# Kernel tuning notes

Measured on AMD Instinct MI355X. Metric: run time of the kernel, lower is better.

Reference implementation:

```python
import math
import jax, jax.numpy as jnp
import numpy as np

B, S, H = 4, 4096, 1024
NH, HD = 16, 64
MLP_DIM = 4096


def _gelu_tanh(x):
    c = math.sqrt(2.0 / math.pi)
    return 0.5 * x * (1.0 + jnp.tanh(c * (x + 0.044715 * x * x * x)))


def _layernorm(x, w, b, eps=1e-5):
    mu = jnp.mean(x, axis=-1, keepdims=True)
    var = jnp.var(x, axis=-1, keepdims=True)
    return (x - mu) * jax.lax.rsqrt(var + eps) * w + b


def setup_inputs() -> dict:
    key = jax.random.key(0)
    ks = jax.random.split(key, 12)
    s = 0.02
    return {
        "x": jax.random.normal(ks[0], (B, S, H), jnp.float32),
        "ln1_w": jnp.ones((H,), jnp.float32),
        "ln1_b": jnp.zeros((H,), jnp.float32),
        "q_w": jax.random.normal(ks[1], (H, H), jnp.float32) * s,
        "q_b": jnp.zeros((H,), jnp.float32),
        "k_w": jax.random.normal(ks[2], (H, H), jnp.float32) * s,
        "k_b": jnp.zeros((H,), jnp.float32),
        "v_w": jax.random.normal(ks[3], (H, H), jnp.float32) * s,
        "v_b": jnp.zeros((H,), jnp.float32),
        "o_w": jax.random.normal(ks[4], (H, H), jnp.float32) * s,
        "o_b": jnp.zeros((H,), jnp.float32),
        "ln2_w": jnp.ones((H,), jnp.float32),
        "ln2_b": jnp.zeros((H,), jnp.float32),
        "fc_w": jax.random.normal(ks[5], (H, MLP_DIM), jnp.float32) * s,
        "fc_b": jnp.zeros((MLP_DIM,), jnp.float32),
        "proj_w": jax.random.normal(ks[6], (MLP_DIM, H), jnp.float32) * (s / math.sqrt(2 * 12)),
        "proj_b": jnp.zeros((H,), jnp.float32),
    }


def reference(x, ln1_w, ln1_b, q_w, q_b, k_w, k_b, v_w, v_b, o_w, o_b,
              ln2_w, ln2_b, fc_w, fc_b, proj_w, proj_b):
    bsz, seqlen, h = x.shape
    ln_x = _layernorm(x, ln1_w, ln1_b)

    # projections -> [b, nh, t, hd]
    def heads(y):
        return y.reshape(bsz, seqlen, NH, HD).transpose(0, 2, 1, 3)

    q = heads(ln_x @ q_w + q_b)
    k = heads(ln_x @ k_w + k_b)
    v = heads(ln_x @ v_w + v_b)

    # feature map: elu(x)+1
    qf = jax.nn.elu(q) + 1.0
    kf = jax.nn.elu(k) + 1.0

    kv = jnp.einsum('bhtd,bhte->bhde', kf, v)              # [b,nh,hd,hd]
    norm = 1.0 / (jnp.einsum('bhtd,bhd->bht', qf, kf.sum(axis=2)) + 1e-6)
    out = jnp.einsum('bhtd,bhde->bhte', qf, kv) * norm[..., None]
    out = out.transpose(0, 2, 1, 3).reshape(bsz, seqlen, h)
    attn = out @ o_w + o_b

    x = x + attn
    h_mlp = _gelu_tanh(_layernorm(x, ln2_w, ln2_b) @ fc_w + fc_b)
    x = x + (h_mlp @ proj_w + proj_b)
    return x
```

## Files before the change

### kernel.cpp

```cpp
#include <hip/hip_runtime.h>
#include <hip/hip_bf16.h>
#include <cstdint>
#include <cstddef>

typedef __bf16 bf16;
typedef __bf16 bf16x8 __attribute__((ext_vector_type(8)));
typedef __bf16 bf16x4 __attribute__((ext_vector_type(4)));
typedef float  f32x4  __attribute__((ext_vector_type(4)));

typedef __attribute__((address_space(1))) void gvoid_t;
typedef __attribute__((address_space(3))) void lvoid_t;

#define GLD_LDS16(g, l) __builtin_amdgcn_global_load_lds( \
    (gvoid_t*)(uintptr_t)(g), (lvoid_t*)(uint32_t)(uintptr_t)(l), 16, 0, 0)

#define SBAR() __builtin_amdgcn_s_barrier()
#define SCHED_FENCE() __builtin_amdgcn_sched_barrier(0)
#define WAIT_VMN(n) asm volatile("s_waitcnt vmcnt(" #n ")" ::: "memory")
#define WAIT_LGKM0() asm volatile("s_waitcnt lgkmcnt(0)" ::: "memory")

__global__ __launch_bounds__(256) void transpose_cast(
    const float* __restrict__ in, bf16* __restrict__ out, int R, int C)
{
  __shared__ float tile[32][33];
  const int bx = blockIdx.x;
  const int by = blockIdx.y;
  const int tx = threadIdx.x;
  const int ty = threadIdx.y;
#pragma unroll
  for (int i = 0; i < 32; i += 8)
    tile[ty + i][tx] = in[(size_t)(by * 32 + ty + i) * C + bx * 32 + tx];
  __syncthreads();
#pragma unroll
  for (int i = 0; i < 32; i += 8)
    out[(size_t)(bx * 32 + ty + i) * R + by * 32 + tx] = (bf16)tile[tx][ty + i];
}

__global__ __launch_bounds__(256) void pack3(
    const float* __restrict__ a, const float* __restrict__ b,
    const float* __restrict__ c, float* __restrict__ o)
{
  const int i = blockIdx.x * 256 + threadIdx.x;
  o[i] = i < 1024 ? a[i] : (i < 2048 ? b[i - 1024] : c[i - 2048]);
}

__global__ __launch_bounds__(256) void ln_row(
    const float* __restrict__ x, const float* __restrict__ w,
    const float* __restrict__ b, bf16* __restrict__ out)
{
  const int row = blockIdx.x;
  const int tid = threadIdx.x;
  const float4 v = ((const float4*)(x + (size_t)row * 1024))[tid];
  float s  = v.x + v.y + v.z + v.w;
  float ss = v.x * v.x + v.y * v.y + v.z * v.z + v.w * v.w;
#pragma unroll
  for (int off = 32; off > 0; off >>= 1) {
    s  += __shfl_down(s, off);
    ss += __shfl_down(ss, off);
  }
  __shared__ float red[8];
  const int wid = tid >> 6, lane = tid & 63;
  if (lane == 0) { red[wid] = s; red[4 + wid] = ss; }
  __syncthreads();
  s  = red[0] + red[1] + red[2] + red[3];
  ss = red[4] + red[5] + red[6] + red[7];
  const float mu   = s * (1.f / 1024.f);
  const float var  = ss * (1.f / 1024.f) - mu * mu;
  const float rstd = rsqrtf(var + 1e-5f);
  const float4 wv = ((const float4*)w)[tid];
  const float4 bv = ((const float4*)b)[tid];
  bf16x4 ov;
  ov[0] = (bf16)((v.x - mu) * rstd * wv.x + bv.x);
  ov[1] = (bf16)((v.y - mu) * rstd * wv.y + bv.y);
  ov[2] = (bf16)((v.z - mu) * rstd * wv.z + bv.z);
  ov[3] = (bf16)((v.w - mu) * rstd * wv.w + bv.w);
  *(bf16x4*)(out + (size_t)row * 1024 + tid * 4) = ov;
}

template <int EPI>
__global__ __launch_bounds__(512, 2) void gemm256(
    const bf16* __restrict__ A, const bf16* __restrict__ BT,
    const float* __restrict__ bias, const float* __restrict__ resid,
    void* __restrict__ outp, int M, int N, int K, int nx)
{
  __shared__ __align__(16) char lds[131072];
  const int tid  = threadIdx.x;
  const int wid  = tid >> 6, lane = tid & 63;
  const int wr   = wid >> 2, wc = wid & 3;
  const int ln15 = lane & 15, lhi = lane >> 4;

  const int nwg = (int)gridDim.x;
  const int cpx = nwg >> 3;
  const int bid = (int)blockIdx.x;
  const int lg  = (bid & 7) * cpx + (bid >> 3);
  const int bx  = lg % nx, by = lg / nx;
  const int row0 = by << 8, col0 = bx << 8;

  const int srowA = tid >> 3;
  const int sslA  = (tid & 7) ^ (srowA & 7);
  const bf16* aS  = A + (size_t)(row0 + srowA) * K + sslA * 8;
  const size_t rjK = (size_t)K << 6;
  const int u8    = tid >> 3, s8 = tid & 7;
  const int gRowB = ((u8 >> 5) << 6) + (u8 & 31);
  const int sslB  = s8 ^ (u8 & 7);
  const bf16* bS  = BT + (size_t)(col0 + gRowB) * K + sslB * 8;

  char* ldsAw = lds + wid * 1024;
  char* ldsBw = lds + 65536 + wid * 1024;

  const int slk0 = (lhi ^ (ln15 & 7)) << 4;
  const int slk1 = ((4 + lhi) ^ (ln15 & 7)) << 4;
  const int rowA0 = ((wr << 7) + ln15) * 128;
  const int rowB0 = 65536 + (wc * 32 + ln15) * 128;

  f32x4 acc[8][4] = {};
  bf16x8 a[4][2], b0[2][2], b1[2][2];
  const int nt = K >> 6;

#define STG_A(D, KT, I) GLD_LDS16(aS + (size_t)(I) * rjK + (size_t)(KT) * 64, \
                                  ldsAw + (D) * 32768 + (I) * 8192)
#define STG_B(D, KT, NH, J) GLD_LDS16(bS + (size_t)((J) * 128 + (NH) * 32) * K + (size_t)(KT) * 64, \
                                      ldsBw + (D) * 32768 + (NH) * 16384 + (J) * 8192)
#define RD_A(D, MH) do { _Pragma("unroll") \
    for (int m_ = 0; m_ < 4; ++m_) { \
      a[m_][0] = *(const bf16x8*)(lds + (D) * 32768 + rowA0 + (MH) * 8192 + m_ * 2048 + slk0); \
      a[m_][1] = *(const bf16x8*)(lds + (D) * 32768 + rowA0 + (MH) * 8192 + m_ * 2048 + slk1); \
    } } while (0)
#define RD_B(D, NH, DST) do { _Pragma("unroll") \
    for (int n_ = 0; n_ < 2; ++n_) { \
      DST[n_][0] = *(const bf16x8*)(lds + (D) * 32768 + rowB0 + (NH) * 16384 + n_ * 2048 + slk0); \
      DST[n_][1] = *(const bf16x8*)(lds + (D) * 32768 + rowB0 + (NH) * 16384 + n_ * 2048 + slk1); \
    } } while (0)
#define MFMA8(MH, NH, BSRC) do { \
    __builtin_amdgcn_s_setprio(1); \
    _Pragma("unroll") for (int m_ = 0; m_ < 4; ++m_) \
    _Pragma("unroll") for (int n_ = 0; n_ < 2; ++n_) { \
      acc[(MH) * 4 + m_][(NH) * 2 + n_] = __builtin_amdgcn_mfma_f32_16x16x32_bf16( \
          a[m_][0], BSRC[n_][0], acc[(MH) * 4 + m_][(NH) * 2 + n_], 0, 0, 0); \
      acc[(MH) * 4 + m_][(NH) * 2 + n_] = __builtin_amdgcn_mfma_f32_16x16x32_bf16( \
          a[m_][1], BSRC[n_][1], acc[(MH) * 4 + m_][(NH) * 2 + n_], 0, 0, 0); \
    } \
    __builtin_amdgcn_s_setprio(0); } while (0)

  STG_A(0, 0, 0); STG_A(0, 0, 2);
  STG_B(0, 0, 0, 0); STG_B(0, 0, 0, 1);
  STG_B(0, 0, 1, 0); STG_B(0, 0, 1, 1);
  STG_A(0, 0, 1); STG_A(0, 0, 3);
  WAIT_VMN(0);
  SBAR(); SCHED_FENCE();

  for (int kt = 0; kt < nt - 1; ++kt) {
    const int d = kt & 1, dn = d ^ 1;
    RD_A(d, 0); RD_B(d, 0, b0);
    STG_A(dn, kt + 1, 0); STG_A(dn, kt + 1, 2);
    SBAR(); WAIT_LGKM0(); SCHED_FENCE();
    MFMA8(0, 0, b0);
    SBAR(); SCHED_FENCE();
    RD_B(d, 1, b1);
    STG_B(dn, kt + 1, 0, 0); STG_B(dn, kt + 1, 0, 1);
    WAIT_VMN(4);
    SBAR(); WAIT_LGKM0(); SCHED_FENCE();
    MFMA8(0, 1, b1);
    SBAR(); SCHED_FENCE();
    RD_A(d, 1);
    STG_B(dn, kt + 1, 1, 0); STG_B(dn, kt + 1, 1, 1);
    SBAR(); WAIT_LGKM0(); SCHED_FENCE();
    MFMA8(1, 0, b0);
    SBAR(); SCHED_FENCE();
    STG_A(dn, kt + 1, 1); STG_A(dn, kt + 1, 3);
    MFMA8(1, 1, b1);
    WAIT_VMN(2);
    SBAR(); SCHED_FENCE();
  }

  {
    const int d = (nt - 1) & 1;
    RD_A(d, 0); RD_B(d, 0, b0);
    SBAR(); WAIT_LGKM0(); SCHED_FENCE();
    MFMA8(0, 0, b0);
    SBAR(); SCHED_FENCE();
    RD_B(d, 1, b1);
    WAIT_VMN(0);
    SBAR(); WAIT_LGKM0(); SCHED_FENCE();
    MFMA8(0, 1, b1);
    SBAR(); SCHED_FENCE();
    RD_A(d, 1);
    WAIT_LGKM0(); SCHED_FENCE();
    MFMA8(1, 0, b0);
    MFMA8(1, 1, b1);
  }
#undef STG_A
#undef STG_B
#undef RD_A
#undef RD_B
#undef MFMA8

  const int lr4 = lhi << 2;
#pragma unroll
  for (int m = 0; m < 8; ++m) {
#pragma unroll
    for (int n = 0; n < 4; ++n) {
      const int c_i = col0 + wc * 64 + n * 16 + ln15;
      const float bv = bias[c_i];
#pragma unroll
      for (int j = 0; j < 4; ++j) {
        const int r_i = row0 + wr * 128 + m * 16 + lr4 + j;
        const size_t idx = (size_t)r_i * N + c_i;
        float val = acc[m][n][j] + bv;
        if constexpr (EPI == 0) {
          ((bf16*)outp)[idx] = (bf16)val;
        } else if constexpr (EPI == 1) {
          ((bf16*)outp)[idx] = (bf16)(val > 0.f ? val + 1.f : __expf(val));
        } else if constexpr (EPI == 2) {
          ((float*)outp)[idx] = val + resid[idx];
        } else if constexpr (EPI == 3) {
          const float u  = 0.7978845608028654f * (val + 0.044715f * val * val * val);
          const float th = 1.f - 2.f / (__expf(2.f * u) + 1.f);
          ((bf16*)outp)[idx] = (bf16)(0.5f * val * (1.f + th));
        } else {
          if (c_i < 2048)
            ((bf16*)outp)[idx] = (bf16)(val > 0.f ? val + 1.f : __expf(val));
          else
            ((bf16*)outp)[idx] = (bf16)val;
        }
      }
    }
  }
}

__global__ __launch_bounds__(256) void kv_part_kernel(
    const bf16* __restrict__ qkv, float* __restrict__ kv_part,
    float* __restrict__ ksum_part)
{
  const int bh = blockIdx.x >> 3, ch = blockIdx.x & 7;
  const int b = bh >> 4, h = bh & 15;
  const int tid = threadIdx.x;
  const int e = tid & 63, dg = tid >> 6;
  const size_t grow0 = (size_t)b * 4096 + (size_t)ch * 512;
  const size_t kbase = 1024 + (size_t)h * 64;
  __shared__ bf16 skf[8][64], sv[8][64];
  float accum[16];
#pragma unroll
  for (int i = 0; i < 16; ++i) accum[i] = 0.f;
  float ks = 0.f;
  const int tt = tid >> 5, cc = (tid & 31) << 1;
  for (int t0 = 0; t0 < 512; t0 += 8) {
    __syncthreads();
    const size_t base = (grow0 + t0 + tt) * 3072 + kbase + cc;
    *(uint32_t*)&skf[tt][cc] = *(const uint32_t*)(qkv + base);
    *(uint32_t*)&sv[tt][cc]  = *(const uint32_t*)(qkv + base + 1024);
    __syncthreads();
#pragma unroll
    for (int q = 0; q < 8; ++q) {
      const float vv = (float)sv[q][e];
#pragma unroll
      for (int dd = 0; dd < 16; ++dd)
        accum[dd] += (float)skf[q][dg * 16 + dd] * vv;
    }
    if (tid < 64) {
#pragma unroll
      for (int q = 0; q < 8; ++q) ks += (float)skf[q][tid];
    }
  }
  float* op = kv_part + (size_t)blockIdx.x * 4096 + (size_t)(dg * 16) * 64 + e;
#pragma unroll
  for (int dd = 0; dd < 16; ++dd) op[dd * 64] = accum[dd];
  if (tid < 64) ksum_part[(size_t)blockIdx.x * 64 + tid] = ks;
}

__global__ __launch_bounds__(256) void kv_reduce(
    const float* __restrict__ kvp, const float* __restrict__ ksp,
    float* __restrict__ kvf, float* __restrict__ ksf)
{
  const int bh = blockIdx.x;
  const int tid = threadIdx.x;
  for (int i = tid; i < 4096; i += 256) {
    float s = 0.f;
#pragma unroll
    for (int ch = 0; ch < 8; ++ch) s += kvp[((size_t)bh * 8 + ch) * 4096 + i];
    kvf[(size_t)bh * 4096 + i] = s;
  }
  if (tid < 64) {
    float s = 0.f;
#pragma unroll
    for (int ch = 0; ch < 8; ++ch) s += ksp[((size_t)bh * 8 + ch) * 64 + tid];
    ksf[(size_t)bh * 64 + tid] = s;
  }
}

__global__ __launch_bounds__(256) void attn_out_kernel(
    const bf16* __restrict__ qkv, const float* __restrict__ kvf,
    const float* __restrict__ ksf, bf16* __restrict__ attn)
{
  const int bh = blockIdx.x >> 6, rb = blockIdx.x & 63;
  const int b = bh >> 4, h = bh & 15;
  const int tid = threadIdx.x;
  const int e = tid & 63, rbase = (tid >> 6) << 4;
  __shared__ __align__(16) bf16 sqf[64][64];
  __shared__ float sks[64];
  const size_t grow0 = (size_t)b * 4096 + (size_t)rb * 64;

  {
    const int rr = tid >> 2, c0 = (tid & 3) << 4;
    const bf16* src = qkv + (grow0 + rr) * 3072 + h * 64 + c0;
    *(bf16x8*)&sqf[rr][c0]     = *(const bf16x8*)src;
    *(bf16x8*)&sqf[rr][c0 + 8] = *(const bf16x8*)(src + 8);
  }
  if (tid < 64) sks[tid] = ksf[(size_t)bh * 64 + tid];

  float kcol[64];
#pragma unroll
  for (int d = 0; d < 64; ++d) kcol[d] = kvf[(size_t)bh * 4096 + d * 64 + e];

  __syncthreads();

  for (int rr = 0; rr < 16; ++rr) {
    const int r = rbase + rr;
    bf16x8 q8[8];
#pragma unroll
    for (int i = 0; i < 8; ++i) q8[i] = *(const bf16x8*)&sqf[r][i * 8];
    float sk = 0.f, sv = 0.f;
#pragma unroll
    for (int i = 0; i < 8; ++i)
#pragma unroll
      for (int jj = 0; jj < 8; ++jj) {
        const float qd = (float)q8[i][jj];
        sk += qd * sks[i * 8 + jj];
        sv += qd * kcol[i * 8 + jj];
      }
    attn[(grow0 + r) * 1024 + h * 64 + e] = (bf16)(sv / (sk + 1e-6f));
  }
}

extern "C" void kernel_launch(void* const* d_in, const int* in_sizes, int n_in,
                              void* d_out, int out_size, void* d_ws, size_t ws_size,
                              hipStream_t stream)
{
  const float* x    = (const float*)d_in[0];
  const float* ln1w = (const float*)d_in[1];
  const float* ln1b = (const float*)d_in[2];
  const float* qw   = (const float*)d_in[3];
  const float* qb   = (const float*)d_in[4];
  const float* kw   = (const float*)d_in[5];
  const float* kb   = (const float*)d_in[6];
  const float* vw   = (const float*)d_in[7];
  const float* vb   = (const float*)d_in[8];
  const float* ow   = (const float*)d_in[9];
  const float* ob   = (const float*)d_in[10];
  const float* ln2w = (const float*)d_in[11];
  const float* ln2b = (const float*)d_in[12];
  const float* fcw  = (const float*)d_in[13];
  const float* fcb  = (const float*)d_in[14];
  const float* pjw  = (const float*)d_in[15];
  const float* pjb  = (const float*)d_in[16];
  float* out = (float*)d_out;
  char* ws = (char*)d_ws;

  constexpr size_t O_LNX  = 0;
  constexpr size_t O_QKV  = 33554432;
  constexpr size_t O_HMLP = 0;
  constexpr size_t O_KVP  = 134217728;
  constexpr size_t O_KSP  = 142606336;
  constexpr size_t O_KVF  = 142737408;
  constexpr size_t O_KSF  = 143785984;
  constexpr size_t O_ATTN = 143802368;
  constexpr size_t O_LN2  = 177356800;
  constexpr size_t O_WQ   = 210911232;
  constexpr size_t O_WO   = 217202688;
  constexpr size_t O_WFC  = 219299840;
  constexpr size_t O_WPJ  = 227688448;

  bf16* lnx   = (bf16*)(ws + O_LNX);
  bf16* qkv   = (bf16*)(ws + O_QKV);
  bf16* hmlp  = (bf16*)(ws + O_HMLP);
  float* kvp  = (float*)(ws + O_KVP);
  float* qkvb = (float*)(ws + O_KVP);
  float* ksp  = (float*)(ws + O_KSP);
  float* kvf  = (float*)(ws + O_KVF);
  float* ksf  = (float*)(ws + O_KSF);
  bf16* attn  = (bf16*)(ws + O_ATTN);
  bf16* ln2h  = (bf16*)(ws + O_LN2);
  bf16* wqkvT = (bf16*)(ws + O_WQ);
  bf16* woT   = (bf16*)(ws + O_WO);
  bf16* wfcT  = (bf16*)(ws + O_WFC);
  bf16* wpjT  = (bf16*)(ws + O_WPJ);

  const dim3 tb(32, 8);
  transpose_cast<<<dim3(32, 32),  tb, 0, stream>>>(qw,  wqkvT,               1024, 1024);
  transpose_cast<<<dim3(32, 32),  tb, 0, stream>>>(kw,  wqkvT + 1024 * 1024, 1024, 1024);
  transpose_cast<<<dim3(32, 32),  tb, 0, stream>>>(vw,  wqkvT + 2048 * 1024, 1024, 1024);
  transpose_cast<<<dim3(32, 32),  tb, 0, stream>>>(ow,  woT, 1024, 1024);
  transpose_cast<<<dim3(128, 32), tb, 0, stream>>>(fcw, wfcT, 1024, 4096);
  transpose_cast<<<dim3(32, 128), tb, 0, stream>>>(pjw, wpjT, 4096, 1024);
  pack3<<<12, 256, 0, stream>>>(qb, kb, vb, qkvb);

  ln_row<<<16384, 256, 0, stream>>>(x, ln1w, ln1b, lnx);

  gemm256<4><<<768, 512, 0, stream>>>(lnx, wqkvT, qkvb, nullptr, qkv, 16384, 3072, 1024, 12);

  kv_part_kernel<<<512, 256, 0, stream>>>(qkv, kvp, ksp);
  kv_reduce<<<64, 256, 0, stream>>>(kvp, ksp, kvf, ksf);
  attn_out_kernel<<<4096, 256, 0, stream>>>(qkv, kvf, ksf, attn);

  gemm256<2><<<256, 512, 0, stream>>>(attn, woT, ob, x, out, 16384, 1024, 1024, 4);

  ln_row<<<16384, 256, 0, stream>>>(out, ln2w, ln2b, ln2h);

  gemm256<3><<<1024, 512, 0, stream>>>(ln2h, wfcT, fcb, nullptr, hmlp, 16384, 4096, 1024, 16);

  gemm256<2><<<256, 512, 0, stream>>>(hmlp, wpjT, pjb, out, out, 16384, 1024, 4096, 4);
}
```

Before: 701.9 us.

## Compute linear-attention output with MFMA using a transposed bf16 KV matrix

Replaces the scalar attn_out kernel with an MFMA kernel. Each wave multiplies a 16-row block of Q features against a bf16 [kv^T | ksum | 0] matrix, so the numerator and normalizer come out of the same matrix multiply. kv_part now accumulates kv transposed and unpacks bf16 pairs by bit shifting, and kv_reduce writes a padded bf16 buffer in place of fp32. The four square weight transposes are merged into one launch. The cost is quantizing kv and ksum to bf16, which adds precision error to the normalizer.

```diff
diff --git a/kernel.cpp b/kernel.cpp
--- a/kernel.cpp
+++ b/kernel.cpp
@@ -19,14 +19,32 @@
 #define WAIT_VMN(n) asm volatile("s_waitcnt vmcnt(" #n ")" ::: "memory")
 #define WAIT_LGKM0() asm volatile("s_waitcnt lgkmcnt(0)" ::: "memory")
 
+__global__ __launch_bounds__(256) void transpose4(
+    const float* __restrict__ qw, const float* __restrict__ kw,
+    const float* __restrict__ vw, const float* __restrict__ ow,
+    bf16* __restrict__ wqkvT, bf16* __restrict__ woT)
+{
+  __shared__ float tile[32][33];
+  const int z = blockIdx.z;
+  const float* in = z == 0 ? qw : (z == 1 ? kw : (z == 2 ? vw : ow));
+  bf16* out = z == 3 ? woT : (wqkvT + (size_t)z * 1024 * 1024);
+  const int bx = blockIdx.x, by = blockIdx.y;
+  const int tx = threadIdx.x, ty = threadIdx.y;
+#pragma unroll
+  for (int i = 0; i < 32; i += 8)
+    tile[ty + i][tx] = in[(size_t)(by * 32 + ty + i) * 1024 + bx * 32 + tx];
+  __syncthreads();
+#pragma unroll
+  for (int i = 0; i < 32; i += 8)
+    out[(size_t)(bx * 32 + ty + i) * 1024 + by * 32 + tx] = (bf16)tile[tx][ty + i];
+}
+
 __global__ __launch_bounds__(256) void transpose_cast(
     const float* __restrict__ in, bf16* __restrict__ out, int R, int C)
 {
   __shared__ float tile[32][33];
-  const int bx = blockIdx.x;
-  const int by = blockIdx.y;
-  const int tx = threadIdx.x;
-  const int ty = threadIdx.y;
+  const int bx = blockIdx.x, by = blockIdx.y;
+  const int tx = threadIdx.x, ty = threadIdx.y;
 #pragma unroll
   for (int i = 0; i < 32; i += 8)
     tile[ty + i][tx] = in[(size_t)(by * 32 + ty + i) * C + bx * 32 + tx];
@@ -235,10 +253,10 @@
   const int bh = blockIdx.x >> 3, ch = blockIdx.x & 7;
   const int b = bh >> 4, h = bh & 15;
   const int tid = threadIdx.x;
-  const int e = tid & 63, dg = tid >> 6;
+  const int d = tid & 63, eg = tid >> 6;
   const size_t grow0 = (size_t)b * 4096 + (size_t)ch * 512;
-  const size_t kbase = 1024 + (size_t)h * 64;
-  __shared__ bf16 skf[8][64], sv[8][64];
+  const size_t vbase = 2048 + (size_t)h * 64;
+  __shared__ bf16 svv[8][64], skf[8][64];
   float accum[16];
 #pragma unroll
   for (int i = 0; i < 16; ++i) accum[i] = 0.f;
@@ -246,89 +264,94 @@
   const int tt = tid >> 5, cc = (tid & 31) << 1;
   for (int t0 = 0; t0 < 512; t0 += 8) {
     __syncthreads();
-    const size_t base = (grow0 + t0 + tt) * 3072 + kbase + cc;
-    *(uint32_t*)&skf[tt][cc] = *(const uint32_t*)(qkv + base);
-    *(uint32_t*)&sv[tt][cc]  = *(const uint32_t*)(qkv + base + 1024);
+    const size_t base = (grow0 + t0 + tt) * 3072 + vbase + cc;
+    *(uint32_t*)&svv[tt][cc] = *(const uint32_t*)(qkv + base);
+    *(uint32_t*)&skf[tt][cc] = *(const uint32_t*)(qkv + base - 1024);
     __syncthreads();
 #pragma unroll
     for (int q = 0; q < 8; ++q) {
-      const float vv = (float)sv[q][e];
-#pragma unroll
-      for (int dd = 0; dd < 16; ++dd)
-        accum[dd] += (float)skf[q][dg * 16 + dd] * vv;
+      const float kd = (float)skf[q][d];
+      const uint32_t* u0 = (const uint32_t*)&svv[q][eg * 16];
+#pragma unroll
+      for (int i = 0; i < 8; ++i) {
+        const uint32_t u = u0[i];
+        const float lo = __uint_as_float(u << 16);
+        const float hi = __uint_as_float(u & 0xffff0000u);
+        accum[2 * i]     += lo * kd;
+        accum[2 * i + 1] += hi * kd;
+      }
     }
     if (tid < 64) {
 #pragma unroll
       for (int q = 0; q < 8; ++q) ks += (float)skf[q][tid];
     }
   }
-  float* op = kv_part + (size_t)blockIdx.x * 4096 + (size_t)(dg * 16) * 64 + e;
-#pragma unroll
-  for (int dd = 0; dd < 16; ++dd) op[dd * 64] = accum[dd];
+  float* op = kv_part + (size_t)blockIdx.x * 4096 + (size_t)(eg * 16) * 64 + d;
+#pragma unroll
+  for (int ee = 0; ee < 16; ++ee) op[ee * 64] = accum[ee];
   if (tid < 64) ksum_part[(size_t)blockIdx.x * 64 + tid] = ks;
 }
 
 __global__ __launch_bounds__(256) void kv_reduce(
     const float* __restrict__ kvp, const float* __restrict__ ksp,
-    float* __restrict__ kvf, float* __restrict__ ksf)
+    bf16* __restrict__ kb)
 {
   const int bh = blockIdx.x;
   const int tid = threadIdx.x;
+  bf16* KB = kb + (size_t)bh * 5120;
   for (int i = tid; i < 4096; i += 256) {
     float s = 0.f;
 #pragma unroll
     for (int ch = 0; ch < 8; ++ch) s += kvp[((size_t)bh * 8 + ch) * 4096 + i];
-    kvf[(size_t)bh * 4096 + i] = s;
+    KB[i] = (bf16)s;
   }
   if (tid < 64) {
     float s = 0.f;
 #pragma unroll
     for (int ch = 0; ch < 8; ++ch) s += ksp[((size_t)bh * 8 + ch) * 64 + tid];
-    ksf[(size_t)bh * 64 + tid] = s;
-  }
-}
-
-__global__ __launch_bounds__(256) void attn_out_kernel(
-    const bf16* __restrict__ qkv, const float* __restrict__ kvf,
-    const float* __restrict__ ksf, bf16* __restrict__ attn)
-{
-  const int bh = blockIdx.x >> 6, rb = blockIdx.x & 63;
+    KB[4096 + tid] = (bf16)s;
+  }
+  for (int i = 4160 + tid; i < 5120; i += 256) KB[i] = (bf16)0.f;
+}
+
+__global__ __launch_bounds__(256) void attn_mfma(
+    const bf16* __restrict__ qkv, const bf16* __restrict__ kb,
+    bf16* __restrict__ attn)
+{
+  const int bh = blockIdx.x >> 4, rb = blockIdx.x & 15;
   const int b = bh >> 4, h = bh & 15;
-  const int tid = threadIdx.x;
-  const int e = tid & 63, rbase = (tid >> 6) << 4;
-  __shared__ __align__(16) bf16 sqf[64][64];
-  __shared__ float sks[64];
-  const size_t grow0 = (size_t)b * 4096 + (size_t)rb * 64;
-
-  {
-    const int rr = tid >> 2, c0 = (tid & 3) << 4;
-    const bf16* src = qkv + (grow0 + rr) * 3072 + h * 64 + c0;
-    *(bf16x8*)&sqf[rr][c0]     = *(const bf16x8*)src;
-    *(bf16x8*)&sqf[rr][c0 + 8] = *(const bf16x8*)(src + 8);
-  }
-  if (tid < 64) sks[tid] = ksf[(size_t)bh * 64 + tid];
-
-  float kcol[64];
-#pragma unroll
-  for (int d = 0; d < 64; ++d) kcol[d] = kvf[(size_t)bh * 4096 + d * 64 + e];
-
-  __syncthreads();
-
-  for (int rr = 0; rr < 16; ++rr) {
-    const int r = rbase + rr;
-    bf16x8 q8[8];
-#pragma unroll
-    for (int i = 0; i < 8; ++i) q8[i] = *(const bf16x8*)&sqf[r][i * 8];
-    float sk = 0.f, sv = 0.f;
-#pragma unroll
-    for (int i = 0; i < 8; ++i)
-#pragma unroll
-      for (int jj = 0; jj < 8; ++jj) {
-        const float qd = (float)q8[i][jj];
-        sk += qd * sks[i * 8 + jj];
-        sv += qd * kcol[i * 8 + jj];
-      }
-    attn[(grow0 + r) * 1024 + h * 64 + e] = (bf16)(sv / (sk + 1e-6f));
+  const int tid = threadIdx.x, wid = tid >> 6, lane = tid & 63;
+  const int ln15 = lane & 15, lhi = lane >> 4;
+  const size_t row0 = (size_t)b * 4096 + rb * 256 + wid * 64;
+  const bf16* KB = kb + (size_t)bh * 5120;
+
+  bf16x8 bfr[5][2];
+#pragma unroll
+  for (int nb = 0; nb < 5; ++nb)
+#pragma unroll
+    for (int ks = 0; ks < 2; ++ks)
+      bfr[nb][ks] = *(const bf16x8*)(KB + (nb * 16 + ln15) * 64 + ks * 32 + lhi * 8);
+
+  for (int mt = 0; mt < 4; ++mt) {
+    const bf16* ap = qkv + (row0 + mt * 16 + ln15) * 3072 + h * 64 + lhi * 8;
+    const bf16x8 a0 = *(const bf16x8*)ap;
+    const bf16x8 a1 = *(const bf16x8*)(ap + 32);
+    f32x4 acc[5];
+#pragma unroll
+    for (int nb = 0; nb < 5; ++nb) {
+      f32x4 z = {0.f, 0.f, 0.f, 0.f};
+      z = __builtin_amdgcn_mfma_f32_16x16x32_bf16(a0, bfr[nb][0], z, 0, 0, 0);
+      acc[nb] = __builtin_amdgcn_mfma_f32_16x16x32_bf16(a1, bfr[nb][1], z, 0, 0, 0);
+    }
+#pragma unroll
+    for (int j = 0; j < 4; ++j) {
+      const float ns = __shfl(acc[4][j], (lane & 48));
+      const float inv = 1.f / (ns + 1e-6f);
+      const size_t r = row0 + mt * 16 + (lhi << 2) + j;
+#pragma unroll
+      for (int nb = 0; nb < 4; ++nb)
+        attn[r * 1024 + h * 64 + nb * 16 + ln15] = (bf16)(acc[nb][j] * inv);
+    }
   }
 }
 
@@ -342,7 +365,7 @@
   const float* qw   = (const float*)d_in[3];
   const float* qb   = (const float*)d_in[4];
   const float* kw   = (const float*)d_in[5];
-  const float* kb   = (const float*)d_in[6];
+  const float* kb_  = (const float*)d_in[6];
   const float* vw   = (const float*)d_in[7];
   const float* vb   = (const float*)d_in[8];
   const float* ow   = (const float*)d_in[9];
@@ -361,8 +384,7 @@
   constexpr size_t O_HMLP = 0;
   constexpr size_t O_KVP  = 134217728;
   constexpr size_t O_KSP  = 142606336;
-  constexpr size_t O_KVF  = 142737408;
-  constexpr size_t O_KSF  = 143785984;
+  constexpr size_t O_KB   = 142737408;
   constexpr size_t O_ATTN = 143802368;
   constexpr size_t O_LN2  = 177356800;
   constexpr size_t O_WQ   = 210911232;
@@ -376,8 +398,7 @@
   float* kvp  = (float*)(ws + O_KVP);
   float* qkvb = (float*)(ws + O_KVP);
   float* ksp  = (float*)(ws + O_KSP);
-  float* kvf  = (float*)(ws + O_KVF);
-  float* ksf  = (float*)(ws + O_KSF);
+  bf16* kbt   = (bf16*)(ws + O_KB);
   bf16* attn  = (bf16*)(ws + O_ATTN);
   bf16* ln2h  = (bf16*)(ws + O_LN2);
   bf16* wqkvT = (bf16*)(ws + O_WQ);
@@ -386,21 +407,18 @@
   bf16* wpjT  = (bf16*)(ws + O_WPJ);
 
   const dim3 tb(32, 8);
-  transpose_cast<<<dim3(32, 32),  tb, 0, stream>>>(qw,  wqkvT,               1024, 1024);
-  transpose_cast<<<dim3(32, 32),  tb, 0, stream>>>(kw,  wqkvT + 1024 * 1024, 1024, 1024);
-  transpose_cast<<<dim3(32, 32),  tb, 0, stream>>>(vw,  wqkvT + 2048 * 1024, 1024, 1024);
-  transpose_cast<<<dim3(32, 32),  tb, 0, stream>>>(ow,  woT, 1024, 1024);
+  transpose4<<<dim3(32, 32, 4), tb, 0, stream>>>(qw, kw, vw, ow, wqkvT, woT);
   transpose_cast<<<dim3(128, 32), tb, 0, stream>>>(fcw, wfcT, 1024, 4096);
   transpose_cast<<<dim3(32, 128), tb, 0, stream>>>(pjw, wpjT, 4096, 1024);
-  pack3<<<12, 256, 0, stream>>>(qb, kb, vb, qkvb);
+  pack3<<<12, 256, 0, stream>>>(qb, kb_, vb, qkvb);
 
   ln_row<<<16384, 256, 0, stream>>>(x, ln1w, ln1b, lnx);
 
   gemm256<4><<<768, 512, 0, stream>>>(lnx, wqkvT, qkvb, nullptr, qkv, 16384, 3072, 1024, 12);
 
   kv_part_kernel<<<512, 256, 0, stream>>>(qkv, kvp, ksp);
-  kv_reduce<<<64, 256, 0, stream>>>(kvp, ksp, kvf, ksf);
-  attn_out_kernel<<<4096, 256, 0, stream>>>(qkv, kvf, ksf, attn);
+  kv_reduce<<<64, 256, 0, stream>>>(kvp, ksp, kbt);
+  attn_mfma<<<1024, 256, 0, stream>>>(qkv, kbt, attn);
 
   gemm256<2><<<256, 512, 0, stream>>>(attn, woT, ob, x, out, 16384, 1024, 1024, 4);
 
```

Measured after the change: 606.3 us, median of 3. 1.16x faster.
